# Optimization experiments

Measured on AMD Instinct MI355X. Metric: run time of the kernel, lower is better.

The kernel has to match this reference:

```python
import jax, jax.numpy as jnp
import numpy as np

S = 2   # scale_factor
K = 5   # k_up
COMP = 64


def setup_inputs() -> dict:
    key = jax.random.key(0)
    k1, k2, k3, k4, k5 = jax.random.split(key, 5)
    B, C, H, W = 2, 256, 64, 64
    x = jax.random.normal(k1, (B, C, H, W), dtype=jnp.float32)
    # content_encoder: 1x1 conv C -> COMP (kaiming fan_out ~ normal * sqrt(2/fan_out))
    w_enc = jax.random.normal(k2, (COMP, C), dtype=jnp.float32) * np.sqrt(2.0 / COMP)
    b_enc = jnp.zeros((COMP,), dtype=jnp.float32)
    # kernel_predictor: 3x3 conv COMP -> S^2*K^2
    KP = S * S * K * K  # 100
    w_kp = jax.random.normal(k3, (KP, COMP, 3, 3), dtype=jnp.float32) * np.sqrt(2.0 / (KP * 9))
    b_kp = jnp.zeros((KP,), dtype=jnp.float32)
    return {"x": x, "w_enc": w_enc, "b_enc": b_enc, "w_kp": w_kp, "b_kp": b_kp}


def reference(x, w_enc, b_enc, w_kp, b_kp):
    B, C, H, W = x.shape
    K2 = K * K
    # content encoder: 1x1 conv
    xc = jnp.einsum('bchw,oc->bohw', x, w_enc) + b_enc[None, :, None, None]
    # kernel predictor: 3x3 conv, padding 1
    k = jax.lax.conv_general_dilated(
        xc, w_kp, window_strides=(1, 1), padding='SAME',
        dimension_numbers=('NCHW', 'OIHW', 'NCHW')) + b_kp[None, :, None, None]
    # pixel_shuffle: [B, K2*S*S, H, W] -> [B, K2, H*S, W*S]
    k = k.reshape(B, K2, S, S, H, W).transpose(0, 1, 4, 2, 5, 3).reshape(B, K2, H * S, W * S)
    k = jax.nn.softmax(k, axis=1)
    # unfold: [B, C, K2, H, W] (dim_proj is Identity since in_channels == out_channels)
    pad = K // 2
    xp = jnp.pad(x, ((0, 0), (0, 0), (pad, pad), (pad, pad)))
    patches = jnp.stack(
        [xp[:, :, i:i + H, j:j + W] for i in range(K) for j in range(K)], axis=2)
    # nearest-neighbor upsample of patches is just indexing the low-res grid:
    # out[b,c,h*S+p,w*S+q] = sum_k patches[b,c,k,h,w] * kernels[b,k,h*S+p,w*S+q]
    kr = k.reshape(B, K2, H, S, W, S)
    out = jnp.einsum('bckhw,bkhpwq->bchpwq', patches, kr)
    return out.reshape(B, C, H * S, W * S)
```

## Files before the change

### kernel.cpp

```cpp
#include <hip/hip_runtime.h>


#define NB 2
#define NC 256

typedef _Float16 h2v __attribute__((ext_vector_type(2)));
typedef __fp16 f16x2 __attribute__((ext_vector_type(2)));
union U32H2 { unsigned u; h2v h; f16x2 f; };
static __device__ __forceinline__ h2v u2h(unsigned u) { U32H2 t; t.u = u; return t.h; }
static __device__ __forceinline__ unsigned pkh(float a, float b) {
    U32H2 t; t.f = __builtin_amdgcn_cvt_pkrtz(a, b); return t.u;
}

__global__ __launch_bounds__(256) void prep_weights(const float* __restrict__ w_kp,
        const float* __restrict__ w_enc, unsigned* __restrict__ whr, float* __restrict__ wt) {
    int idx = blockIdx.x * 256 + threadIdx.x;
    if (idx < 32256) {
        int k = idx % 28;
        int d = (idx / 28) % 9;
        int cp = (idx / 252) % 32;
        int g = idx / 8064;
        unsigned val = 0;
        if (k < 25) {
            float a = w_kp[((size_t)(k * 4 + g) * 64 + 2 * cp) * 9 + d];
            float b = w_kp[((size_t)(k * 4 + g) * 64 + 2 * cp + 1) * 9 + d];
            val = pkh(a, b);
        }
        whr[idx] = val;
    }
    int j = idx - 32256;
    if (j >= 0 && j < 16384) {
        int o32 = j % 32;
        int c = (j / 32) % 256;
        int half = j / 8192;
        wt[j] = w_enc[(half * 32 + o32) * 256 + c];
    }
}

__global__ __launch_bounds__(512) void encoder_kernel(const float* __restrict__ x,
        const float* __restrict__ wt, const float* __restrict__ b_enc,
        unsigned* __restrict__ xch) {
    __shared__ float xs[256 * 64];
    int bid = blockIdx.x;
    int half = bid & 1;
    int h = (bid >> 1) & 63;
    int b = bid >> 7;
    int tid = threadIdx.x;
    for (int i = 0; i < 32; ++i) {
        int f = i * 512 + tid;
        int c = f >> 6, w = f & 63;
        xs[f] = x[((size_t)(b * NC + c)) * 4096 + h * 64 + w];
    }
    __syncthreads();
    int wl = tid & 63;
    int og = __builtin_amdgcn_readfirstlane(tid >> 6);
    const float* wrow = wt + half * 8192 + og * 4;
    float a0 = 0.f, a1 = 0.f, a2 = 0.f, a3 = 0.f;
#pragma unroll 8
    for (int c = 0; c < 256; ++c) {
        float xv = xs[c * 64 + wl];
        const float* wp = wrow + c * 32;
        a0 = fmaf(xv, wp[0], a0);
        a1 = fmaf(xv, wp[1], a1);
        a2 = fmaf(xv, wp[2], a2);
        a3 = fmaf(xv, wp[3], a3);
    }
    int o0 = half * 32 + og * 4;
    a0 += b_enc[o0 + 0]; a1 += b_enc[o0 + 1]; a2 += b_enc[o0 + 2]; a3 += b_enc[o0 + 3];
    int cp0 = o0 >> 1;
    xch[((size_t)(b * 32 + cp0)) * 4096 + h * 64 + wl]     = pkh(a0, a1);
    xch[((size_t)(b * 32 + cp0 + 1)) * 4096 + h * 64 + wl] = pkh(a2, a3);
}

__global__ __launch_bounds__(256) void kp_conv_kernel(const unsigned* __restrict__ xch,
        const unsigned* __restrict__ whr, const float* __restrict__ b_kp,
        unsigned* __restrict__ kerh) {
    __shared__ unsigned xcs[3840];
    __shared__ float red[6400];
    int bid = blockIdx.x;
    int g = bid & 3;
    int tile = (bid >> 2) & 63;
    int b = bid >> 8;
    int trow = tile >> 3, tcol = tile & 7;
    int tid = threadIdx.x;
    for (int i = 0; i < 15; ++i) {
        int f = i * 256 + tid;
        if (f < 3840) {
            int s = f % 12;
            int r = (f / 12) % 10;
            int cp = f / 120;
            unsigned v = 0;
            int gh = trow * 8 + r - 1, gw = tcol * 8 + s - 1;
            if (s < 10 && gh >= 0 && gh < 64 && gw >= 0 && gw < 64)
                v = xch[((size_t)(b * 32 + cp)) * 4096 + gh * 64 + gw];
            xcs[f] = v;
        }
    }
    __syncthreads();
    int lane = tid & 63;
    int coq = __builtin_amdgcn_readfirstlane(tid >> 6);
    int hy = lane >> 3, hx = lane & 7;
    float acc[25];
#pragma unroll
    for (int k = 0; k < 25; ++k) acc[k] = 0.f;
    const unsigned* wg = whr + g * 8064 + coq * 8 * 252;
#pragma unroll 1
    for (int ci = 0; ci < 8; ++ci) {
        int cp = coq * 8 + ci;
        const unsigned* xb = xcs + cp * 120 + hy * 12 + hx;
        unsigned xwin[9];
#pragma unroll
        for (int di = 0; di < 3; ++di)
#pragma unroll
            for (int dj = 0; dj < 3; ++dj)
                xwin[di * 3 + dj] = xb[di * 12 + dj];
        const unsigned* wp = wg + ci * 252;
#pragma unroll
        for (int d = 0; d < 9; ++d) {
            h2v xv = u2h(xwin[d]);
#pragma unroll
            for (int k = 0; k < 25; ++k)
                acc[k] = __builtin_amdgcn_fdot2(xv, u2h(wp[d * 28 + k]), acc[k], false);
        }
    }
#pragma unroll
    for (int k = 0; k < 25; ++k) red[coq * 1600 + k * 64 + lane] = acc[k];
    __syncthreads();
    if (coq == 0) {
        float l[25];
#pragma unroll
        for (int k = 0; k < 25; ++k)
            l[k] = red[k * 64 + lane] + red[1600 + k * 64 + lane]
                 + red[3200 + k * 64 + lane] + red[4800 + k * 64 + lane]
                 + b_kp[k * 4 + g];
        float m = l[0];
#pragma unroll
        for (int k = 1; k < 25; ++k) m = fmaxf(m, l[k]);
        float s = 0.f;
#pragma unroll
        for (int k = 0; k < 25; ++k) { l[k] = __expf(l[k] - m); s += l[k]; }
        float inv = 1.f / s;
#pragma unroll
        for (int k = 0; k < 25; ++k) l[k] *= inv;
        int t = trow * 4 + (tcol >> 1);
        int lg = hy * 8 + (tcol & 1) * 4 + (hx >> 1);
        int pxsel = hx & 1;
        unsigned* kb = kerh + ((size_t)((b * 32 + t) * 2 + pxsel)) * 3840 + lg;
#pragma unroll
        for (int i = 0; i < 5; ++i) {
            unsigned u0 = pkh(l[i * 5 + 0], l[i * 5 + 1]);
            unsigned u1 = pkh(l[i * 5 + 2], l[i * 5 + 3]);
            unsigned u2 = pxsel ? pkh(0.f, l[i * 5 + 4]) : pkh(l[i * 5 + 4], 0.f);
            kb[((g * 5 + i) * 3 + 0) * 64] = u0;
            kb[((g * 5 + i) * 3 + 1) * 64] = u1;
            kb[((g * 5 + i) * 3 + 2) * 64] = u2;
        }
    }
}

__global__ __launch_bounds__(256) void gather_kernel(const float* __restrict__ x,
        const unsigned* __restrict__ kerh, float* __restrict__ out) {
    __shared__ unsigned xs[16 * 132];
    int bid = blockIdx.x;
    int cblk = bid & 15;
    int t = (bid >> 4) & 31;
    int b = bid >> 9;
    int ty = t >> 2, tx = t & 3;
    int c0 = cblk * 16;
    int tid = threadIdx.x;
    for (int i = 0; i < 8; ++i) {
        int f = i * 256 + tid;
        if (f < 1920) {
            int p = f % 10;
            int r = (f / 10) % 12;
            int ch = f / 120;
            int gh = ty * 8 + r - 2;
            int gw = tx * 16 + 2 * p - 2;
            float v0 = 0.f, v1 = 0.f;
            if (gh >= 0 && gh < 64) {
                const float* xp = x + ((size_t)(b * NC + c0 + ch)) * 4096 + gh * 64;
                if (gw >= 0 && gw < 64) v0 = xp[gw];
                if (gw + 1 >= 0 && gw + 1 < 64) v1 = xp[gw + 1];
            }
            xs[ch * 132 + r * 11 + p] = pkh(v0, v1);
        }
    }
    __syncthreads();
    int lane = tid & 63;
    int wid = tid >> 6;
    int hy = lane >> 3, hxp = lane & 7;
    const unsigned* kb0 = kerh + ((size_t)(b * 32 + t) * 2) * 3840 + lane;
    const unsigned* kb1 = kb0 + 3840;
    unsigned wv[4][5][3];
    float r0[4][4], r1[4][4];
#pragma unroll
    for (int g = 0; g < 4; ++g)
#pragma unroll
        for (int i = 0; i < 5; ++i)
#pragma unroll
            for (int j = 0; j < 3; ++j)
                wv[g][i][j] = kb0[((g * 5 + i) * 3 + j) * 64];
#pragma unroll
    for (int ch = 0; ch < 4; ++ch) {
        const unsigned* xb = xs + (wid * 4 + ch) * 132 + hy * 11 + hxp;
        float a0 = 0.f, a1 = 0.f, a2 = 0.f, a3 = 0.f;
#pragma unroll
        for (int i = 0; i < 5; ++i) {
            unsigned A = xb[i * 11], B = xb[i * 11 + 1], C = xb[i * 11 + 2];
            a0 = __builtin_amdgcn_fdot2(u2h(A), u2h(wv[0][i][0]), a0, false);
            a0 = __builtin_amdgcn_fdot2(u2h(B), u2h(wv[0][i][1]), a0, false);
            a0 = __builtin_amdgcn_fdot2(u2h(C), u2h(wv[0][i][2]), a0, false);
            a1 = __builtin_amdgcn_fdot2(u2h(A), u2h(wv[1][i][0]), a1, false);
            a1 = __builtin_amdgcn_fdot2(u2h(B), u2h(wv[1][i][1]), a1, false);
            a1 = __builtin_amdgcn_fdot2(u2h(C), u2h(wv[1][i][2]), a1, false);
            a2 = __builtin_amdgcn_fdot2(u2h(A), u2h(wv[2][i][0]), a2, false);
            a2 = __builtin_amdgcn_fdot2(u2h(B), u2h(wv[2][i][1]), a2, false);
            a2 = __builtin_amdgcn_fdot2(u2h(C), u2h(wv[2][i][2]), a2, false);
            a3 = __builtin_amdgcn_fdot2(u2h(A), u2h(wv[3][i][0]), a3, false);
            a3 = __builtin_amdgcn_fdot2(u2h(B), u2h(wv[3][i][1]), a3, false);
            a3 = __builtin_amdgcn_fdot2(u2h(C), u2h(wv[3][i][2]), a3, false);
        }
        r0[ch][0] = a0; r0[ch][1] = a1; r0[ch][2] = a2; r0[ch][3] = a3;
    }
#pragma unroll
    for (int g = 0; g < 4; ++g)
#pragma unroll
        for (int i = 0; i < 5; ++i)
#pragma unroll
            for (int j = 0; j < 3; ++j)
                wv[g][i][j] = kb1[((g * 5 + i) * 3 + j) * 64];
#pragma unroll
    for (int ch = 0; ch < 4; ++ch) {
        const unsigned* xb = xs + (wid * 4 + ch) * 132 + hy * 11 + hxp;
        float a0 = 0.f, a1 = 0.f, a2 = 0.f, a3 = 0.f;
#pragma unroll
        for (int i = 0; i < 5; ++i) {
            unsigned A = xb[i * 11], B = xb[i * 11 + 1], C = xb[i * 11 + 2];
            unsigned P1 = (A >> 16) | (B << 16);
            unsigned P2 = (B >> 16) | (C << 16);
            a0 = __builtin_amdgcn_fdot2(u2h(P1), u2h(wv[0][i][0]), a0, false);
            a0 = __builtin_amdgcn_fdot2(u2h(P2), u2h(wv[0][i][1]), a0, false);
            a0 = __builtin_amdgcn_fdot2(u2h(C),  u2h(wv[0][i][2]), a0, false);
            a1 = __builtin_amdgcn_fdot2(u2h(P1), u2h(wv[1][i][0]), a1, false);
            a1 = __builtin_amdgcn_fdot2(u2h(P2), u2h(wv[1][i][1]), a1, false);
            a1 = __builtin_amdgcn_fdot2(u2h(C),  u2h(wv[1][i][2]), a1, false);
            a2 = __builtin_amdgcn_fdot2(u2h(P1), u2h(wv[2][i][0]), a2, false);
            a2 = __builtin_amdgcn_fdot2(u2h(P2), u2h(wv[2][i][1]), a2, false);
            a2 = __builtin_amdgcn_fdot2(u2h(C),  u2h(wv[2][i][2]), a2, false);
            a3 = __builtin_amdgcn_fdot2(u2h(P1), u2h(wv[3][i][0]), a3, false);
            a3 = __builtin_amdgcn_fdot2(u2h(P2), u2h(wv[3][i][1]), a3, false);
            a3 = __builtin_amdgcn_fdot2(u2h(C),  u2h(wv[3][i][2]), a3, false);
        }
        r1[ch][0] = a0; r1[ch][1] = a1; r1[ch][2] = a2; r1[ch][3] = a3;
    }
    int oy0 = (ty * 8 + hy) * 2;
    int ox0 = tx * 32 + 4 * hxp;
#pragma unroll
    for (int ch = 0; ch < 4; ++ch) {
        int cc = c0 + wid * 4 + ch;
        float* rb = out + ((size_t)(b * NC + cc) * 128 + oy0) * 128 + ox0;
        *reinterpret_cast<float4*>(rb)       = make_float4(r0[ch][0], r0[ch][1], r1[ch][0], r1[ch][1]);
        *reinterpret_cast<float4*>(rb + 128) = make_float4(r0[ch][2], r0[ch][3], r1[ch][2], r1[ch][3]);
    }
}

extern "C" void kernel_launch(void* const* d_in, const int* in_sizes, int n_in,
                              void* d_out, int out_size, void* d_ws, size_t ws_size,
                              hipStream_t stream) {
    const float* x     = (const float*)d_in[0];
    const float* w_enc = (const float*)d_in[1];
    const float* b_enc = (const float*)d_in[2];
    const float* w_kp  = (const float*)d_in[3];
    const float* b_kp  = (const float*)d_in[4];
    float* out = (float*)d_out;

    float* wt = (float*)d_ws;
    unsigned* whr  = (unsigned*)(wt + 16384);
    unsigned* xch  = whr + 32256;
    unsigned* kerh = xch + 262144;

    prep_weights<<<190, 256, 0, stream>>>(w_kp, w_enc, whr, wt);
    encoder_kernel<<<256, 512, 0, stream>>>(x, wt, b_enc, xch);
    kp_conv_kernel<<<512, 256, 0, stream>>>(xch, whr, b_kp, kerh);
    gather_kernel<<<1024, 256, 0, stream>>>(x, kerh, out);
}
```

Measured before the change: 69.17 us.

## Fold weight prep into encoder, vectorize loads, spread softmax, double gather channels

Removes the separate prep_weights launch. The first 63 encoder blocks now repack the kp-conv weights, and the encoder reads w_enc directly instead of a transposed copy. The encoder loads x with float4 and remaps block indices so the two halves of a row land on different blocks. In kp_conv the softmax epilogue is computed by all four waves rather than one, though only the first 16 lanes of each wave write results. The gather kernel handles 32 channels per block with half as many blocks, reusing the loaded kernel weights across more channels at the cost of more registers and LDS.

```diff
diff --git a/kernel.cpp b/kernel.cpp
--- a/kernel.cpp
+++ b/kernel.cpp
@@ -12,58 +12,53 @@
     U32H2 t; t.f = __builtin_amdgcn_cvt_pkrtz(a, b); return t.u;
 }
 
-__global__ __launch_bounds__(256) void prep_weights(const float* __restrict__ w_kp,
-        const float* __restrict__ w_enc, unsigned* __restrict__ whr, float* __restrict__ wt) {
-    int idx = blockIdx.x * 256 + threadIdx.x;
-    if (idx < 32256) {
-        int k = idx % 28;
-        int d = (idx / 28) % 9;
-        int cp = (idx / 252) % 32;
-        int g = idx / 8064;
-        unsigned val = 0;
-        if (k < 25) {
-            float a = w_kp[((size_t)(k * 4 + g) * 64 + 2 * cp) * 9 + d];
-            float b = w_kp[((size_t)(k * 4 + g) * 64 + 2 * cp + 1) * 9 + d];
-            val = pkh(a, b);
-        }
-        whr[idx] = val;
-    }
-    int j = idx - 32256;
-    if (j >= 0 && j < 16384) {
-        int o32 = j % 32;
-        int c = (j / 32) % 256;
-        int half = j / 8192;
-        wt[j] = w_enc[(half * 32 + o32) * 256 + c];
-    }
-}
-
 __global__ __launch_bounds__(512) void encoder_kernel(const float* __restrict__ x,
-        const float* __restrict__ wt, const float* __restrict__ b_enc,
-        unsigned* __restrict__ xch) {
+        const float* __restrict__ w_enc, const float* __restrict__ b_enc,
+        const float* __restrict__ w_kp, unsigned* __restrict__ xch,
+        unsigned* __restrict__ whr) {
     __shared__ float xs[256 * 64];
     int bid = blockIdx.x;
-    int half = bid & 1;
-    int h = (bid >> 1) & 63;
     int b = bid >> 7;
+    int hi = (bid >> 4) & 7;
+    int half = (bid >> 3) & 1;
+    int lo = bid & 7;
+    int h = hi * 8 + lo;
     int tid = threadIdx.x;
-    for (int i = 0; i < 32; ++i) {
+    if (bid < 63) {
+        int idx = bid * 512 + tid;
+        if (idx < 32256) {
+            int k = idx % 28;
+            int d = (idx / 28) % 9;
+            int cp = (idx / 252) % 32;
+            int g = idx / 8064;
+            unsigned val = 0;
+            if (k < 25) {
+                float a = w_kp[((size_t)(k * 4 + g) * 64 + 2 * cp) * 9 + d];
+                float bb = w_kp[((size_t)(k * 4 + g) * 64 + 2 * cp + 1) * 9 + d];
+                val = pkh(a, bb);
+            }
+            whr[idx] = val;
+        }
+    }
+    const float* xb = x + ((size_t)(b * NC)) * 4096 + h * 64;
+    for (int i = 0; i < 8; ++i) {
         int f = i * 512 + tid;
-        int c = f >> 6, w = f & 63;
-        xs[f] = x[((size_t)(b * NC + c)) * 4096 + h * 64 + w];
+        int c = f >> 4, w4 = f & 15;
+        *reinterpret_cast<float4*>(xs + c * 64 + w4 * 4) =
+            *reinterpret_cast<const float4*>(xb + (size_t)c * 4096 + w4 * 4);
     }
     __syncthreads();
     int wl = tid & 63;
     int og = __builtin_amdgcn_readfirstlane(tid >> 6);
-    const float* wrow = wt + half * 8192 + og * 4;
+    const float* w0 = w_enc + (size_t)(half * 32 + og * 4) * 256;
     float a0 = 0.f, a1 = 0.f, a2 = 0.f, a3 = 0.f;
 #pragma unroll 8
     for (int c = 0; c < 256; ++c) {
         float xv = xs[c * 64 + wl];
-        const float* wp = wrow + c * 32;
-        a0 = fmaf(xv, wp[0], a0);
-        a1 = fmaf(xv, wp[1], a1);
-        a2 = fmaf(xv, wp[2], a2);
-        a3 = fmaf(xv, wp[3], a3);
+        a0 = fmaf(xv, w0[c], a0);
+        a1 = fmaf(xv, w0[256 + c], a1);
+        a2 = fmaf(xv, w0[512 + c], a2);
+        a3 = fmaf(xv, w0[768 + c], a3);
     }
     int o0 = half * 32 + og * 4;
     a0 += b_enc[o0 + 0]; a1 += b_enc[o0 + 1]; a2 += b_enc[o0 + 2]; a3 += b_enc[o0 + 3];
@@ -126,12 +121,13 @@
 #pragma unroll
     for (int k = 0; k < 25; ++k) red[coq * 1600 + k * 64 + lane] = acc[k];
     __syncthreads();
-    if (coq == 0) {
+    {
+        int px = coq * 16 + (lane & 15);
         float l[25];
 #pragma unroll
         for (int k = 0; k < 25; ++k)
-            l[k] = red[k * 64 + lane] + red[1600 + k * 64 + lane]
-                 + red[3200 + k * 64 + lane] + red[4800 + k * 64 + lane]
+            l[k] = red[k * 64 + px] + red[1600 + k * 64 + px]
+                 + red[3200 + k * 64 + px] + red[4800 + k * 64 + px]
                  + b_kp[k * 4 + g];
         float m = l[0];
 #pragma unroll
@@ -142,35 +138,38 @@
         float inv = 1.f / s;
 #pragma unroll
         for (int k = 0; k < 25; ++k) l[k] *= inv;
+        int phy = px >> 3, phx = px & 7;
         int t = trow * 4 + (tcol >> 1);
-        int lg = hy * 8 + (tcol & 1) * 4 + (hx >> 1);
-        int pxsel = hx & 1;
+        int lg = phy * 8 + (tcol & 1) * 4 + (phx >> 1);
+        int pxsel = phx & 1;
         unsigned* kb = kerh + ((size_t)((b * 32 + t) * 2 + pxsel)) * 3840 + lg;
-#pragma unroll
-        for (int i = 0; i < 5; ++i) {
-            unsigned u0 = pkh(l[i * 5 + 0], l[i * 5 + 1]);
-            unsigned u1 = pkh(l[i * 5 + 2], l[i * 5 + 3]);
-            unsigned u2 = pxsel ? pkh(0.f, l[i * 5 + 4]) : pkh(l[i * 5 + 4], 0.f);
-            kb[((g * 5 + i) * 3 + 0) * 64] = u0;
-            kb[((g * 5 + i) * 3 + 1) * 64] = u1;
-            kb[((g * 5 + i) * 3 + 2) * 64] = u2;
+        if ((lane >> 4) == 0) {
+#pragma unroll
+            for (int i = 0; i < 5; ++i) {
+                unsigned u0 = pkh(l[i * 5 + 0], l[i * 5 + 1]);
+                unsigned u1 = pkh(l[i * 5 + 2], l[i * 5 + 3]);
+                unsigned u2 = pxsel ? pkh(0.f, l[i * 5 + 4]) : pkh(l[i * 5 + 4], 0.f);
+                kb[((g * 5 + i) * 3 + 0) * 64] = u0;
+                kb[((g * 5 + i) * 3 + 1) * 64] = u1;
+                kb[((g * 5 + i) * 3 + 2) * 64] = u2;
+            }
         }
     }
 }
 
 __global__ __launch_bounds__(256) void gather_kernel(const float* __restrict__ x,
         const unsigned* __restrict__ kerh, float* __restrict__ out) {
-    __shared__ unsigned xs[16 * 132];
+    __shared__ unsigned xs[32 * 132];
     int bid = blockIdx.x;
-    int cblk = bid & 15;
-    int t = (bid >> 4) & 31;
-    int b = bid >> 9;
+    int cblk = bid & 7;
+    int t = (bid >> 3) & 31;
+    int b = bid >> 8;
     int ty = t >> 2, tx = t & 3;
-    int c0 = cblk * 16;
+    int c0 = cblk * 32;
     int tid = threadIdx.x;
-    for (int i = 0; i < 8; ++i) {
+    for (int i = 0; i < 15; ++i) {
         int f = i * 256 + tid;
-        if (f < 1920) {
+        if (f < 3840) {
             int p = f % 10;
             int r = (f / 10) % 12;
             int ch = f / 120;
@@ -192,7 +191,7 @@
     const unsigned* kb0 = kerh + ((size_t)(b * 32 + t) * 2) * 3840 + lane;
     const unsigned* kb1 = kb0 + 3840;
     unsigned wv[4][5][3];
-    float r0[4][4], r1[4][4];
+    float r0[8][4], r1[8][4];
 #pragma unroll
     for (int g = 0; g < 4; ++g)
 #pragma unroll
@@ -201,8 +200,8 @@
             for (int j = 0; j < 3; ++j)
                 wv[g][i][j] = kb0[((g * 5 + i) * 3 + j) * 64];
 #pragma unroll
-    for (int ch = 0; ch < 4; ++ch) {
-        const unsigned* xb = xs + (wid * 4 + ch) * 132 + hy * 11 + hxp;
+    for (int ch = 0; ch < 8; ++ch) {
+        const unsigned* xb = xs + (wid * 8 + ch) * 132 + hy * 11 + hxp;
         float a0 = 0.f, a1 = 0.f, a2 = 0.f, a3 = 0.f;
 #pragma unroll
         for (int i = 0; i < 5; ++i) {
@@ -230,8 +229,8 @@
             for (int j = 0; j < 3; ++j)
                 wv[g][i][j] = kb1[((g * 5 + i) * 3 + j) * 64];
 #pragma unroll
-    for (int ch = 0; ch < 4; ++ch) {
-        const unsigned* xb = xs + (wid * 4 + ch) * 132 + hy * 11 + hxp;
+    for (int ch = 0; ch < 8; ++ch) {
+        const unsigned* xb = xs + (wid * 8 + ch) * 132 + hy * 11 + hxp;
         float a0 = 0.f, a1 = 0.f, a2 = 0.f, a3 = 0.f;
 #pragma unroll
         for (int i = 0; i < 5; ++i) {
@@ -256,8 +255,8 @@
     int oy0 = (ty * 8 + hy) * 2;
     int ox0 = tx * 32 + 4 * hxp;
 #pragma unroll
-    for (int ch = 0; ch < 4; ++ch) {
-        int cc = c0 + wid * 4 + ch;
+    for (int ch = 0; ch < 8; ++ch) {
+        int cc = c0 + wid * 8 + ch;
         float* rb = out + ((size_t)(b * NC + cc) * 128 + oy0) * 128 + ox0;
         *reinterpret_cast<float4*>(rb)       = make_float4(r0[ch][0], r0[ch][1], r1[ch][0], r1[ch][1]);
         *reinterpret_cast<float4*>(rb + 128) = make_float4(r0[ch][2], r0[ch][3], r1[ch][2], r1[ch][3]);
@@ -274,13 +273,11 @@
     const float* b_kp  = (const float*)d_in[4];
     float* out = (float*)d_out;
 
-    float* wt = (float*)d_ws;
-    unsigned* whr  = (unsigned*)(wt + 16384);
+    unsigned* whr  = (unsigned*)d_ws;
     unsigned* xch  = whr + 32256;
     unsigned* kerh = xch + 262144;
 
-    prep_weights<<<190, 256, 0, stream>>>(w_kp, w_enc, whr, wt);
-    encoder_kernel<<<256, 512, 0, stream>>>(x, wt, b_enc, xch);
+    encoder_kernel<<<256, 512, 0, stream>>>(x, w_enc, b_enc, w_kp, xch, whr);
     kp_conv_kernel<<<512, 256, 0, stream>>>(xch, whr, b_kp, kerh);
-    gather_kernel<<<1024, 256, 0, stream>>>(x, kerh, out);
-}
+    gather_kernel<<<512, 256, 0, stream>>>(x, kerh, out);
+}
```

New measurement: 55.77 us. 19.4% less time.
